# Optimization experiments

Measured on AMD Instinct MI355X. Metric: run time of the kernel, lower is better.

## Reference

```python
import jax, jax.numpy as jnp
import numpy as np

N_NODES = 200000
N_ETYPES = 4
N_EDGES = 500000
D_IN = 128
D_OUT = 128


def setup_inputs() -> dict:
    key = jax.random.key(0)
    ks = jax.random.split(key, 7)
    scale = 1.0 / np.sqrt(D_IN)
    x = jax.random.normal(ks[0], (N_NODES, D_IN), dtype=jnp.float32)
    W = jax.random.normal(ks[1], (N_ETYPES, D_IN, D_OUT), dtype=jnp.float32) * scale
    b = jax.random.normal(ks[2], (N_ETYPES, D_OUT), dtype=jnp.float32) * 0.01
    W_self = jax.random.normal(ks[3], (D_IN, D_OUT), dtype=jnp.float32) * scale
    b_self = jax.random.normal(ks[4], (D_OUT,), dtype=jnp.float32) * 0.01
    src = jax.random.randint(ks[5], (N_ETYPES, N_EDGES), 0, N_NODES, dtype=jnp.int32)
    dst = jax.random.randint(ks[6], (N_ETYPES, N_EDGES), 0, N_NODES, dtype=jnp.int32)
    return {"x": x, "W": W, "b": b, "W_self": W_self, "b_self": b_self,
            "src": src, "dst": dst}


def _etype_mean_agg(Wx_e, src_e, dst_e, n_nodes):
    # gather transformed src features along edges, mean-reduce per dst node
    m = Wx_e[src_e]  # [E, d_out]
    s = jax.ops.segment_sum(m, dst_e, num_segments=n_nodes)  # [N, d_out]
    cnt = jax.ops.segment_sum(jnp.ones((src_e.shape[0],), dtype=Wx_e.dtype),
                              dst_e, num_segments=n_nodes)  # [N]
    # nodes with no in-edges of this etype contribute 0 (DGL leaves h unset -> 0)
    return jnp.where(cnt[:, None] > 0, s / jnp.maximum(cnt[:, None], 1.0), 0.0)


def reference(x, W, b, W_self, b_self, src, dst):
    n_nodes = x.shape[0]
    # per-etype linear transform of all node features: [T, N, d_out]
    Wx = jnp.einsum('nd,tdf->tnf', x, W) + b[:, None, :]
    # per-etype gather + segment mean, then sum across etypes ('sum' cross-reducer)
    h = jax.vmap(_etype_mean_agg, in_axes=(0, 0, 0, None))(Wx, src, dst, n_nodes)
    h = h.sum(axis=0)  # [N, d_out]
    self_msg = x @ W_self + b_self
    return self_msg + h
```

## Files before the change

kernel.cpp:

```cpp
#include <hip/hip_runtime.h>
#include <hip/hip_bf16.h>


namespace {

constexpr int N  = 200000;
constexpr int T  = 4;
constexpr int E  = 500000;
constexpr int D  = 128;
constexpr int NT = 64;
constexpr int AS = 136;

constexpr int CNT_B = (T * E / 4 + 255) / 256;
constexpr int PX_B  = (N * D / 8) / 256;
constexpr int PW_B  = (5 * D * D / 8 + 255) / 256;
constexpr int SC_B  = (T * E / 4 + 255) / 256;

typedef __bf16 bf16x8 __attribute__((ext_vector_type(8)));
typedef float  f32x4  __attribute__((ext_vector_type(4)));

__global__ void k_zero(int* __restrict__ p, int n) {
  int i = blockIdx.x * 256 + threadIdx.x;
  int4 z = {0, 0, 0, 0};
  if (i * 4 + 3 < n) {
    *(int4*)(p + i * 4) = z;
  } else {
    for (int j = i * 4; j < n; ++j) p[j] = 0;
  }
}

template <bool XB>
__global__ void k_prep(const int* __restrict__ dst, int* __restrict__ cnt,
                       int* __restrict__ rank, const float* __restrict__ x,
                       __bf16* __restrict__ xb, const float* __restrict__ W,
                       const float* __restrict__ Wself, __bf16* __restrict__ wt) {
  const int bid = blockIdx.x;
  const int tid = threadIdx.x;
  if (bid < CNT_B) {
    int i0 = (bid * 256 + tid) * 4;
    if (i0 < T * E) {
      int t = i0 / E;
      int4 d = *(const int4*)(dst + i0);
      int4 r;
      r.x = atomicAdd(&cnt[t * N + d.x], 1);
      r.y = atomicAdd(&cnt[t * N + d.y], 1);
      r.z = atomicAdd(&cnt[t * N + d.z], 1);
      r.w = atomicAdd(&cnt[t * N + d.w], 1);
      *(int4*)(rank + i0) = r;
    }
  } else if (XB && bid < CNT_B + PX_B) {
    int i = (bid - CNT_B) * 256 + tid;
    if (i < N * D / 8) {
      const float4* xs = (const float4*)(x + i * 8);
      float4 a = xs[0], c = xs[1];
      bf16x8 v;
      v[0] = (__bf16)a.x; v[1] = (__bf16)a.y; v[2] = (__bf16)a.z; v[3] = (__bf16)a.w;
      v[4] = (__bf16)c.x; v[5] = (__bf16)c.y; v[6] = (__bf16)c.z; v[7] = (__bf16)c.w;
      *(bf16x8*)(xb + i * 8) = v;
    }
  } else {
    int i = (bid - CNT_B - (XB ? PX_B : 0)) * 256 + tid;
    if (i < 5 * D * D / 8) {
      int base = i * 8;
      int p = base >> 14, rem = base & 16383;
      int n = rem >> 7, k0 = rem & 127;
      const float* Wsrc = (p < 4) ? (W + (size_t)p * D * D) : Wself;
      bf16x8 v;
#pragma unroll
      for (int j = 0; j < 8; ++j) v[j] = (__bf16)Wsrc[(k0 + j) * D + n];
      *(bf16x8*)(wt + base) = v;
    }
  }
}

__global__ void k_offsets(const int* __restrict__ cnt, int* __restrict__ offs,
                          int* __restrict__ cursor) {
  __shared__ int s[256];
  __shared__ int base;
  int tid = threadIdx.x;
  int i = blockIdx.x * 256 + tid;
  int c = (i < T * N) ? cnt[i] : 0;
  s[tid] = c;
  __syncthreads();
  for (int d = 1; d < 256; d <<= 1) {
    int v = (tid >= d) ? s[tid - d] : 0;
    __syncthreads();
    s[tid] += v;
    __syncthreads();
  }
  if (tid == 255) base = atomicAdd(cursor, s[255]);
  __syncthreads();
  if (i < T * N) offs[i] = base + s[tid] - c;
}

__global__ void k_scatter(const int* __restrict__ src, const int* __restrict__ dst,
                          const int* __restrict__ offs, const int* __restrict__ rank,
                          int* __restrict__ eid) {
  int i0 = (blockIdx.x * 256 + threadIdx.x) * 4;
  if (i0 >= T * E) return;
  const int tb = (i0 / E) * N;
  int4 s = *(const int4*)(src + i0);
  int4 d = *(const int4*)(dst + i0);
  int4 r = *(const int4*)(rank + i0);
  eid[offs[tb + d.x] + r.x] = s.x;
  eid[offs[tb + d.y] + r.y] = s.y;
  eid[offs[tb + d.z] + r.z] = s.z;
  eid[offs[tb + d.w] + r.w] = s.w;
}

template <bool XB>
__global__ __launch_bounds__(256, 3) void k_fused(
    const float* __restrict__ x, const __bf16* __restrict__ xb,
    const __bf16* __restrict__ wt, const float* __restrict__ b,
    const float* __restrict__ bself, const int* __restrict__ cnt,
    const int* __restrict__ offs, const int* __restrict__ eid,
    float* __restrict__ out) {
  __shared__ __align__(16) __bf16 a_s[NT * AS];
  __shared__ __align__(16) __bf16 w_s[D * AS];

  const int tid  = threadIdx.x;
  const int nb   = blockIdx.x * NT;
  const int wv   = tid >> 6;
  const int lane = tid & 63;
  const int quad = lane >> 4;
  const int l16  = lane & 15;
  const int ln   = tid >> 2;
  const int q    = tid & 3;

  f32x4 acc[8];
#pragma unroll
  for (int ct = 0; ct < 8; ++ct) acc[ct] = (f32x4){0.f, 0.f, 0.f, 0.f};

  for (int pass = 0; pass < 5; ++pass) {
    const bool self = (pass == 4);

    {
      const __bf16* wsrc = wt + pass * D * D;
#pragma unroll
      for (int c = 0; c < 8; ++c) {
        int idx  = c * 256 + tid;
        int row  = idx >> 4;
        int col8 = (idx & 15) * 8;
        *(bf16x8*)(w_s + row * AS + col8) = *(const bf16x8*)(wsrc + row * D + col8);
      }
    }

    if (!(XB && self)) {
      float r[32];
#pragma unroll
      for (int i = 0; i < 32; ++i) r[i] = 0.f;
      const int node = nb + ln;
      if (self) {
        const float4* xr = (const float4*)(x + node * D + q * 32);
#pragma unroll
        for (int i = 0; i < 8; ++i) {
          float4 v = xr[i];
          r[4 * i] = v.x; r[4 * i + 1] = v.y; r[4 * i + 2] = v.z; r[4 * i + 3] = v.w;
        }
      } else {
        const int base = offs[pass * N + node];
        const int deg  = cnt[pass * N + node];
        int nxt = (deg > 0) ? eid[base] : 0;
        for (int e = 0; e < deg; ++e) {
          const int sidx = nxt;
          nxt = eid[base + e + 1];
          if (XB) {
            const bf16x8* xr = (const bf16x8*)(xb + sidx * D + q * 32);
            bf16x8 v0 = xr[0], v1 = xr[1], v2 = xr[2], v3 = xr[3];
#pragma unroll
            for (int j = 0; j < 8; ++j) {
              r[j]      += (float)v0[j];
              r[8 + j]  += (float)v1[j];
              r[16 + j] += (float)v2[j];
              r[24 + j] += (float)v3[j];
            }
          } else {
            const float4* xr = (const float4*)(x + sidx * D + q * 32);
#pragma unroll
            for (int i = 0; i < 8; ++i) {
              float4 v = xr[i];
              r[4 * i] += v.x; r[4 * i + 1] += v.y;
              r[4 * i + 2] += v.z; r[4 * i + 3] += v.w;
            }
          }
        }
        const float inv = (deg > 0) ? (1.0f / (float)deg) : 0.0f;
#pragma unroll
        for (int i = 0; i < 32; ++i) r[i] *= inv;
      }
      __bf16* arow = a_s + ln * AS + q * 32;
#pragma unroll
      for (int g = 0; g < 4; ++g) {
        bf16x8 v;
#pragma unroll
        for (int j = 0; j < 8; ++j) v[j] = (__bf16)r[8 * g + j];
        *(bf16x8*)(arow + g * 8) = v;
      }
    }
    __syncthreads();

#pragma unroll
    for (int ks = 0; ks < 4; ++ks) {
      bf16x8 af;
      if (XB && self) {
        af = *(const bf16x8*)(xb + (nb + 16 * wv + l16) * D + ks * 32 + quad * 8);
      } else {
        af = *(const bf16x8*)(a_s + (16 * wv + l16) * AS + ks * 32 + quad * 8);
      }
#pragma unroll
      for (int ct = 0; ct < 8; ++ct) {
        bf16x8 bfr = *(const bf16x8*)(w_s + (16 * ct + l16) * AS + ks * 32 + quad * 8);
        acc[ct] = __builtin_amdgcn_mfma_f32_16x16x32_bf16(af, bfr, acc[ct], 0, 0, 0);
      }
    }

    {
      const float* bt = self ? bself : (b + pass * D);
      bool rowon[4];
#pragma unroll
      for (int r = 0; r < 4; ++r) {
        rowon[r] = self ? true : (cnt[pass * N + nb + 16 * wv + quad * 4 + r] > 0);
      }
#pragma unroll
      for (int ct = 0; ct < 8; ++ct) {
        float bv = bt[16 * ct + l16];
#pragma unroll
        for (int r = 0; r < 4; ++r)
          if (rowon[r]) acc[ct][r] += bv;
      }
    }
    if (pass < 4) __syncthreads();
  }

#pragma unroll
  for (int ct = 0; ct < 8; ++ct) {
#pragma unroll
    for (int r = 0; r < 4; ++r) {
      out[(nb + 16 * wv + quad * 4 + r) * D + 16 * ct + l16] = acc[ct][r];
    }
  }
}

}

extern "C" void kernel_launch(void* const* d_in, const int* in_sizes, int n_in,
                              void* d_out, int out_size, void* d_ws, size_t ws_size,
                              hipStream_t stream) {
  const float* x     = (const float*)d_in[0];
  const float* W     = (const float*)d_in[1];
  const float* b     = (const float*)d_in[2];
  const float* Wself = (const float*)d_in[3];
  const float* bself = (const float*)d_in[4];
  const int*   src   = (const int*)d_in[5];
  const int*   dst   = (const int*)d_in[6];
  float* out = (float*)d_out;

  int* cnt    = (int*)d_ws;
  int* cursor = cnt + T * N;
  int* offs   = cursor + 4;
  int* eid    = offs + T * N;
  int* rank   = eid + T * E;
  __bf16* wt  = (__bf16*)(rank + T * E);
  __bf16* xb  = wt + 5 * D * D;

  const size_t need_xb =
      (size_t)(T * N + 4 + T * N + T * E + T * E) * 4 + (size_t)5 * D * D * 2 +
      (size_t)N * D * 2;
  const bool use_xb = ws_size >= need_xb;

  k_zero<<<(T * N + 4 + 1023) / 1024, 256, 0, stream>>>(cnt, T * N + 4);
  if (use_xb) {
    k_prep<true><<<CNT_B + PX_B + PW_B, 256, 0, stream>>>(dst, cnt, rank, x, xb,
                                                          W, Wself, wt);
  } else {
    k_prep<false><<<CNT_B + PW_B, 256, 0, stream>>>(dst, cnt, rank, x, xb, W,
                                                    Wself, wt);
  }
  k_offsets<<<(T * N + 255) / 256, 256, 0, stream>>>(cnt, offs, cursor);
  k_scatter<<<SC_B, 256, 0, stream>>>(src, dst, offs, rank, eid);
  if (use_xb) {
    k_fused<true><<<N / NT, 256, 0, stream>>>(x, xb, wt, b, bself, cnt, offs,
                                              eid, out);
  } else {
    k_fused<false><<<N / NT, 256, 0, stream>>>(x, xb, wt, b, bself, cnt, offs,
                                               eid, out);
  }
}
```

Baseline: 539.3 us.

## Shard degree-count atomics into 8 copies and software-pipeline neighbor gathers

```diff
diff --git a/kernel.cpp b/kernel.cpp
--- a/kernel.cpp
+++ b/kernel.cpp
@@ -10,27 +10,17 @@
 constexpr int D  = 128;
 constexpr int NT = 64;
 constexpr int AS = 136;
+constexpr int TN = T * N;
 
 constexpr int CNT_B = (T * E / 4 + 255) / 256;
 constexpr int PX_B  = (N * D / 8) / 256;
 constexpr int PW_B  = (5 * D * D / 8 + 255) / 256;
-constexpr int SC_B  = (T * E / 4 + 255) / 256;
 
 typedef __bf16 bf16x8 __attribute__((ext_vector_type(8)));
 typedef float  f32x4  __attribute__((ext_vector_type(4)));
 
-__global__ void k_zero(int* __restrict__ p, int n) {
-  int i = blockIdx.x * 256 + threadIdx.x;
-  int4 z = {0, 0, 0, 0};
-  if (i * 4 + 3 < n) {
-    *(int4*)(p + i * 4) = z;
-  } else {
-    for (int j = i * 4; j < n; ++j) p[j] = 0;
-  }
-}
-
-template <bool XB>
-__global__ void k_prep(const int* __restrict__ dst, int* __restrict__ cnt,
+template <bool SH>
+__global__ void k_prep(const int* __restrict__ dst, int* __restrict__ cnt_s,
                        int* __restrict__ rank, const float* __restrict__ x,
                        __bf16* __restrict__ xb, const float* __restrict__ W,
                        const float* __restrict__ Wself, __bf16* __restrict__ wt) {
@@ -42,13 +32,23 @@
       int t = i0 / E;
       int4 d = *(const int4*)(dst + i0);
       int4 r;
-      r.x = atomicAdd(&cnt[t * N + d.x], 1);
-      r.y = atomicAdd(&cnt[t * N + d.y], 1);
-      r.z = atomicAdd(&cnt[t * N + d.z], 1);
-      r.w = atomicAdd(&cnt[t * N + d.w], 1);
+      if (SH) {
+        const int sh = bid & 7;
+        int* mc = cnt_s + sh * TN + t * N;
+        r.x = atomicAdd(&mc[d.x], 1) | (sh << 28);
+        r.y = atomicAdd(&mc[d.y], 1) | (sh << 28);
+        r.z = atomicAdd(&mc[d.z], 1) | (sh << 28);
+        r.w = atomicAdd(&mc[d.w], 1) | (sh << 28);
+      } else {
+        int* mc = cnt_s + t * N;
+        r.x = atomicAdd(&mc[d.x], 1);
+        r.y = atomicAdd(&mc[d.y], 1);
+        r.z = atomicAdd(&mc[d.z], 1);
+        r.w = atomicAdd(&mc[d.w], 1);
+      }
       *(int4*)(rank + i0) = r;
     }
-  } else if (XB && bid < CNT_B + PX_B) {
+  } else if (bid < CNT_B + PX_B) {
     int i = (bid - CNT_B) * 256 + tid;
     if (i < N * D / 8) {
       const float4* xs = (const float4*)(x + i * 8);
@@ -59,7 +59,7 @@
       *(bf16x8*)(xb + i * 8) = v;
     }
   } else {
-    int i = (bid - CNT_B - (XB ? PX_B : 0)) * 256 + tid;
+    int i = (bid - CNT_B - PX_B) * 256 + tid;
     if (i < 5 * D * D / 8) {
       int base = i * 8;
       int p = base >> 14, rem = base & 16383;
@@ -73,13 +73,68 @@
   }
 }
 
+__global__ void k_offsets_sh(const int* __restrict__ cnt_s, int* __restrict__ offs,
+                             int* __restrict__ cnt_tot, int* __restrict__ sbase,
+                             int* __restrict__ cursor) {
+  __shared__ int s[256];
+  __shared__ int base;
+  int tid = threadIdx.x;
+  int i = blockIdx.x * 256 + tid;
+  int c[8];
+  int tot = 0;
+#pragma unroll
+  for (int k = 0; k < 8; ++k) { c[k] = cnt_s[k * TN + i]; tot += c[k]; }
+  s[tid] = tot;
+  __syncthreads();
+  for (int d2 = 1; d2 < 256; d2 <<= 1) {
+    int v = (tid >= d2) ? s[tid - d2] : 0;
+    __syncthreads();
+    s[tid] += v;
+    __syncthreads();
+  }
+  if (tid == 255) base = atomicAdd(cursor, s[255]);
+  __syncthreads();
+  int a = base + s[tid] - tot;
+  offs[i] = a;
+  cnt_tot[i] = tot;
+#pragma unroll
+  for (int k = 0; k < 8; ++k) { sbase[k * TN + i] = a; a += c[k]; }
+}
+
+__global__ void k_scatter_sh(const int* __restrict__ src, const int* __restrict__ dst,
+                             const int* __restrict__ sbase,
+                             const int* __restrict__ rank, int* __restrict__ eid) {
+  int i0 = (blockIdx.x * 256 + threadIdx.x) * 4;
+  if (i0 >= T * E) return;
+  const int tb = (i0 / E) * N;
+  int4 sv = *(const int4*)(src + i0);
+  int4 d  = *(const int4*)(dst + i0);
+  int4 rp = *(const int4*)(rank + i0);
+  {
+    unsigned u = (unsigned)rp.x;
+    eid[sbase[(u >> 28) * TN + tb + d.x] + (int)(u & 0x0FFFFFFFu)] = sv.x;
+  }
+  {
+    unsigned u = (unsigned)rp.y;
+    eid[sbase[(u >> 28) * TN + tb + d.y] + (int)(u & 0x0FFFFFFFu)] = sv.y;
+  }
+  {
+    unsigned u = (unsigned)rp.z;
+    eid[sbase[(u >> 28) * TN + tb + d.z] + (int)(u & 0x0FFFFFFFu)] = sv.z;
+  }
+  {
+    unsigned u = (unsigned)rp.w;
+    eid[sbase[(u >> 28) * TN + tb + d.w] + (int)(u & 0x0FFFFFFFu)] = sv.w;
+  }
+}
+
 __global__ void k_offsets(const int* __restrict__ cnt, int* __restrict__ offs,
                           int* __restrict__ cursor) {
   __shared__ int s[256];
   __shared__ int base;
   int tid = threadIdx.x;
   int i = blockIdx.x * 256 + tid;
-  int c = (i < T * N) ? cnt[i] : 0;
+  int c = (i < TN) ? cnt[i] : 0;
   s[tid] = c;
   __syncthreads();
   for (int d = 1; d < 256; d <<= 1) {
@@ -90,7 +145,7 @@
   }
   if (tid == 255) base = atomicAdd(cursor, s[255]);
   __syncthreads();
-  if (i < T * N) offs[i] = base + s[tid] - c;
+  if (i < TN) offs[i] = base + s[tid] - c;
 }
 
 __global__ void k_scatter(const int* __restrict__ src, const int* __restrict__ dst,
@@ -151,31 +206,43 @@
       for (int i = 0; i < 32; ++i) r[i] = 0.f;
       const int node = nb + ln;
       if (self) {
-        const float4* xr = (const float4*)(x + node * D + q * 32);
+        const float4* xr = (const float4*)(x + (size_t)node * D + q * 32);
 #pragma unroll
         for (int i = 0; i < 8; ++i) {
           float4 v = xr[i];
           r[4 * i] = v.x; r[4 * i + 1] = v.y; r[4 * i + 2] = v.z; r[4 * i + 3] = v.w;
         }
       } else {
+        const int deg  = cnt[pass * N + node];
         const int base = offs[pass * N + node];
-        const int deg  = cnt[pass * N + node];
-        int nxt = (deg > 0) ? eid[base] : 0;
-        for (int e = 0; e < deg; ++e) {
-          const int sidx = nxt;
-          nxt = eid[base + e + 1];
-          if (XB) {
-            const bf16x8* xr = (const bf16x8*)(xb + sidx * D + q * 32);
+        if (XB) {
+          if (deg > 0) {
+            int nxt = eid[base];
+            const bf16x8* xr = (const bf16x8*)(xb + (size_t)nxt * D + q * 32);
             bf16x8 v0 = xr[0], v1 = xr[1], v2 = xr[2], v3 = xr[3];
-#pragma unroll
-            for (int j = 0; j < 8; ++j) {
-              r[j]      += (float)v0[j];
-              r[8 + j]  += (float)v1[j];
-              r[16 + j] += (float)v2[j];
-              r[24 + j] += (float)v3[j];
+            for (int e = 0; e < deg; ++e) {
+              bf16x8 w0, w1, w2, w3;
+              if (e + 1 < deg) {
+                int nx2 = eid[base + e + 1];
+                const bf16x8* x2 = (const bf16x8*)(xb + (size_t)nx2 * D + q * 32);
+                w0 = x2[0]; w1 = x2[1]; w2 = x2[2]; w3 = x2[3];
+              } else {
+                w0 = v0; w1 = v1; w2 = v2; w3 = v3;
+              }
+#pragma unroll
+              for (int j = 0; j < 8; ++j) {
+                r[j]      += (float)v0[j];
+                r[8 + j]  += (float)v1[j];
+                r[16 + j] += (float)v2[j];
+                r[24 + j] += (float)v3[j];
+              }
+              v0 = w0; v1 = w1; v2 = w2; v3 = w3;
             }
-          } else {
-            const float4* xr = (const float4*)(x + sidx * D + q * 32);
+          }
+        } else {
+          for (int e = 0; e < deg; ++e) {
+            const int sidx = eid[base + e];
+            const float4* xr = (const float4*)(x + (size_t)sidx * D + q * 32);
 #pragma unroll
             for (int i = 0; i < 8; ++i) {
               float4 v = xr[i];
@@ -203,7 +270,8 @@
     for (int ks = 0; ks < 4; ++ks) {
       bf16x8 af;
       if (XB && self) {
-        af = *(const bf16x8*)(xb + (nb + 16 * wv + l16) * D + ks * 32 + quad * 8);
+        af = *(const bf16x8*)(xb + (size_t)(nb + 16 * wv + l16) * D + ks * 32 +
+                              quad * 8);
       } else {
         af = *(const bf16x8*)(a_s + (16 * wv + l16) * AS + ks * 32 + quad * 8);
       }
@@ -236,7 +304,7 @@
   for (int ct = 0; ct < 8; ++ct) {
 #pragma unroll
     for (int r = 0; r < 4; ++r) {
-      out[(nb + 16 * wv + quad * 4 + r) * D + 16 * ct + l16] = acc[ct][r];
+      out[(size_t)(nb + 16 * wv + quad * 4 + r) * D + 16 * ct + l16] = acc[ct][r];
     }
   }
 }
@@ -255,34 +323,48 @@
   const int*   dst   = (const int*)d_in[6];
   float* out = (float*)d_out;
 
+  const size_t need_sh =
+      (size_t)(8 * TN + 4 + TN + TN + 8 * TN + T * E + T * E) * 4 +
+      (size_t)5 * D * D * 2 + (size_t)N * D * 2;
+  const size_t need_fb =
+      (size_t)(TN + 4 + TN + T * E + T * E) * 4 + (size_t)5 * D * D * 2 +
+      (size_t)N * D * 2;
+
+  if (ws_size >= need_sh) {
+    int* cnt_s  = (int*)d_ws;
+    int* cursor = cnt_s + 8 * TN;
+    int* offs   = cursor + 4;
+    int* cnt_t  = offs + TN;
+    int* sbase  = cnt_t + TN;
+    int* eid    = sbase + 8 * TN;
+    int* rank   = eid + T * E;
+    __bf16* wt  = (__bf16*)(rank + T * E);
+    __bf16* xb  = wt + 5 * D * D;
+
+    hipMemsetAsync(cnt_s, 0, (size_t)(8 * TN + 4) * 4, stream);
+    k_prep<true><<<CNT_B + PX_B + PW_B, 256, 0, stream>>>(dst, cnt_s, rank, x, xb,
+                                                          W, Wself, wt);
+    k_offsets_sh<<<TN / 256, 256, 0, stream>>>(cnt_s, offs, cnt_t, sbase, cursor);
+    k_scatter_sh<<<CNT_B, 256, 0, stream>>>(src, dst, sbase, rank, eid);
+    k_fused<true><<<N / NT, 256, 0, stream>>>(x, xb, wt, b, bself, cnt_t, offs,
+                                              eid, out);
+    return;
+  }
+
   int* cnt    = (int*)d_ws;
-  int* cursor = cnt + T * N;
+  int* cursor = cnt + TN;
   int* offs   = cursor + 4;
-  int* eid    = offs + T * N;
+  int* eid    = offs + TN;
   int* rank   = eid + T * E;
   __bf16* wt  = (__bf16*)(rank + T * E);
   __bf16* xb  = wt + 5 * D * D;
-
-  const size_t need_xb =
-      (size_t)(T * N + 4 + T * N + T * E + T * E) * 4 + (size_t)5 * D * D * 2 +
-      (size_t)N * D * 2;
-  const bool use_xb = ws_size >= need_xb;
-
-  k_zero<<<(T * N + 4 + 1023) / 1024, 256, 0, stream>>>(cnt, T * N + 4);
-  if (use_xb) {
-    k_prep<true><<<CNT_B + PX_B + PW_B, 256, 0, stream>>>(dst, cnt, rank, x, xb,
-                                                          W, Wself, wt);
-  } else {
-    k_prep<false><<<CNT_B + PW_B, 256, 0, stream>>>(dst, cnt, rank, x, xb, W,
-                                                    Wself, wt);
-  }
-  k_offsets<<<(T * N + 255) / 256, 256, 0, stream>>>(cnt, offs, cursor);
-  k_scatter<<<SC_B, 256, 0, stream>>>(src, dst, offs, rank, eid);
-  if (use_xb) {
-    k_fused<true><<<N / NT, 256, 0, stream>>>(x, xb, wt, b, bself, cnt, offs,
-                                              eid, out);
-  } else {
-    k_fused<false><<<N / NT, 256, 0, stream>>>(x, xb, wt, b, bself, cnt, offs,
-                                               eid, out);
-  }
-}
+  (void)need_fb;
+
+  hipMemsetAsync(cnt, 0, (size_t)(TN + 4) * 4, stream);
+  k_prep<false><<<CNT_B + PX_B + PW_B, 256, 0, stream>>>(dst, cnt, rank, x, xb,
+                                                         W, Wself, wt);
+  k_offsets<<<(TN + 255) / 256, 256, 0, stream>>>(cnt, offs, cursor);
+  k_scatter<<<CNT_B, 256, 0, stream>>>(src, dst, offs, rank, eid);
+  k_fused<true><<<N / NT, 256, 0, stream>>>(x, xb, wt, b, bself, cnt, offs,
+                                            eid, out);
+}
```

After: 538.1 us. About the same (-0.2%).
